# Performance work log

Measured on AMD Instinct MI355X. Metric: run time of the kernel, lower is better.

The kernel has to match this reference:

```python
import jax, jax.numpy as jnp
import numpy as np

B, T, C = 2, 2048, 2048
N_HEAD, N_KV_HEAD = 16, 4
HEAD_DIM = C // N_HEAD  # 128
HALF = HEAD_DIM // 2    # 64


def _rms_norm(x):
    # F.rms_norm with no weight: x / sqrt(mean(x^2) + eps), eps = dtype eps
    eps = jnp.finfo(x.dtype).eps
    return x * jax.lax.rsqrt(jnp.mean(x * x, axis=-1, keepdims=True) + eps)


def _rope_apply(x, cos, sin):
    # x: [B, H, T, Hs]; cos/sin: [1, 1, T, Hs/2]
    x1, x2 = x[..., :HALF], x[..., HALF:]
    return jnp.concatenate([x1 * cos - x2 * sin, x1 * sin + x2 * cos], axis=-1)


def setup_inputs() -> dict:
    key = jax.random.key(0)
    ks = jax.random.split(key, 8)
    x = jax.random.normal(ks[0], (B, T, C), dtype=jnp.float32)
    # real RoPE tables (base 10000), shape [1,1,T,HALF]
    inv_freq = 1.0 / (10000.0 ** (np.arange(0, HALF, dtype=np.float32) / HALF))
    t = np.arange(T, dtype=np.float32)
    ang = np.einsum('t,f->tf', t, inv_freq)
    cos = jnp.asarray(np.cos(ang))[None, None]
    sin = jnp.asarray(np.sin(ang))[None, None]
    s = 0.02
    Wq = jax.random.normal(ks[1], (C, N_HEAD * HEAD_DIM), dtype=jnp.float32) * s
    Wk = jax.random.normal(ks[2], (C, N_KV_HEAD * HEAD_DIM), dtype=jnp.float32) * s
    Wv = jax.random.normal(ks[3], (C, N_KV_HEAD * HEAD_DIM), dtype=jnp.float32) * s
    Wo = jax.random.normal(ks[4], (C, C), dtype=jnp.float32) * s
    bo = jnp.zeros((C,), dtype=jnp.float32)
    return {"x": x, "cos": cos, "sin": sin, "Wq": Wq, "Wk": Wk, "Wv": Wv, "Wo": Wo, "bo": bo}


def reference(x, cos, sin, Wq, Wk, Wv, Wo, bo):
    Bq, Tq, Cq = x.shape
    G = N_HEAD // N_KV_HEAD
    # QKV projections (GQA, no bias)
    q = (x @ Wq).reshape(Bq, Tq, N_HEAD, HEAD_DIM)
    k = (x @ Wk).reshape(Bq, Tq, N_KV_HEAD, HEAD_DIM)
    v = (x @ Wv).reshape(Bq, Tq, N_KV_HEAD, HEAD_DIM)
    # QK RMSNorm (over head_dim), then to [B, H, T, Hs]
    q = jnp.transpose(_rms_norm(q), (0, 2, 1, 3))
    k = jnp.transpose(_rms_norm(k), (0, 2, 1, 3))
    v = jnp.transpose(v, (0, 2, 1, 3))
    # RoPE
    q = _rope_apply(q, cos[:, :, :Tq, :], sin[:, :, :Tq, :])
    k = _rope_apply(k, cos[:, :, :Tq, :], sin[:, :, :Tq, :])
    # GQA: repeat kv heads across groups
    k = jnp.repeat(k, G, axis=1)  # [B, H, T, Hs]
    v = jnp.repeat(v, G, axis=1)
    # Causal SDPA
    scale = 1.0 / jnp.sqrt(jnp.asarray(HEAD_DIM, dtype=x.dtype))
    scores = jnp.einsum('bhqd,bhkd->bhqk', q, k) * scale
    causal = jnp.tril(jnp.ones((Tq, Tq), dtype=bool))
    scores = jnp.where(causal, scores, jnp.asarray(-jnp.inf, dtype=scores.dtype))
    attn = jax.nn.softmax(scores, axis=-1)
    y = jnp.einsum('bhqk,bhkd->bhqd', attn, v)
    y = jnp.transpose(y, (0, 2, 1, 3)).reshape(Bq, Tq, Cq)
    return y @ Wo + bo
```

## Files before the change

kernel.cpp:

```cpp
#include <hip/hip_runtime.h>
#include <hip/hip_bf16.h>
#include <math.h>

#define BB 2
#define TT 2048
#define CC 2048
#define NH 16
#define NKV 4
#define HD 128
#define HALF 64
#define MTOT (BB*TT)
#define NQKV (CC + 2*NKV*HD)

typedef unsigned short u16;
typedef __attribute__((ext_vector_type(8))) short bf16x8;
typedef __attribute__((ext_vector_type(4))) float f32x4;

__device__ __forceinline__ u16 f2bf(float f) {
  unsigned u = __float_as_uint(f);
  unsigned r = (u + 0x7FFFu + ((u >> 16) & 1u)) >> 16;
  return (u16)r;
}
__device__ __forceinline__ float bf2f(u16 v) {
  return __uint_as_float(((unsigned)v) << 16);
}

__device__ __forceinline__ void gl_lds16(const void* g, void* l) {
  __builtin_amdgcn_global_load_lds(
      (const __attribute__((address_space(1))) unsigned int*)g,
      (__attribute__((address_space(3))) unsigned int*)l, 16, 0, 0);
}

__global__ __launch_bounds__(256) void prep(
    const float* __restrict__ x, const float* __restrict__ Wq,
    const float* __restrict__ Wk, const float* __restrict__ Wv,
    const float* __restrict__ Wo, u16* __restrict__ xb,
    u16* __restrict__ Wt, u16* __restrict__ Wot) {
  const int z = blockIdx.z;
  const int tx = threadIdx.x, ty = threadIdx.y;
  if (z == 4) {
    const int tid = ty * 32 + tx;
    const int i = (blockIdx.y * 64 + blockIdx.x) * 256 + tid;
    const float4* s4 = (const float4*)x;
    float4 a = s4[(size_t)i * 2], b = s4[(size_t)i * 2 + 1];
    bf16x8 o;
    o[0] = (short)f2bf(a.x); o[1] = (short)f2bf(a.y);
    o[2] = (short)f2bf(a.z); o[3] = (short)f2bf(a.w);
    o[4] = (short)f2bf(b.x); o[5] = (short)f2bf(b.y);
    o[6] = (short)f2bf(b.z); o[7] = (short)f2bf(b.w);
    ((bf16x8*)xb)[i] = o;
    return;
  }
  const float* W; u16* dst; int N; int row_off;
  if (z == 0)      { W = Wq; dst = Wt;  N = 2048; row_off = 0; }
  else if (z == 1) { W = Wk; dst = Wt;  N = 512;  row_off = 2048; }
  else if (z == 2) { W = Wv; dst = Wt;  N = 512;  row_off = 2560; }
  else             { W = Wo; dst = Wot; N = 2048; row_off = 0; }
  const int n0 = blockIdx.x * 32, k0 = blockIdx.y * 32;
  if (n0 >= N) return;
  __shared__ float tile[32][33];
#pragma unroll
  for (int i = 0; i < 4; ++i)
    tile[ty + 8 * i][tx] = W[(size_t)(k0 + ty + 8 * i) * N + n0 + tx];
  __syncthreads();
#pragma unroll
  for (int i = 0; i < 4; ++i)
    dst[(size_t)(row_off + n0 + ty + 8 * i) * CC + k0 + tx] =
        f2bf(tile[tx][ty + 8 * i]);
}

__global__ __launch_bounds__(256) void gemm_bt_bf16(
    const u16* __restrict__ A, const u16* __restrict__ Bt,
    const float* __restrict__ bias, float* __restrict__ C,
    int M, int N, int K, int out_bf16) {
  __shared__ u16 As[128 * 32];
  __shared__ u16 Bs[128 * 32];
  const int tid = threadIdx.x;
  const int wave = tid >> 6, lane = tid & 63;
  const int quad = lane >> 4, lo = lane & 15;
  const int bm = blockIdx.y * 128, bn = blockIdx.x * 128;
  const int wm = (wave & 1) * 64, wn = (wave >> 1) * 64;

  f32x4 acc[4][4];
#pragma unroll
  for (int i = 0; i < 4; ++i)
#pragma unroll
    for (int j = 0; j < 4; ++j)
#pragma unroll
      for (int r = 0; r < 4; ++r) acc[i][j][r] = 0.f;

  const int iss0 = wave * 2, iss1 = wave * 2 + 1;
  const int e0 = iss0 * 512 + lane * 8, e1 = iss1 * 512 + lane * 8;
  const int r0 = e0 >> 5, c0 = e0 & 31;
  const int r1 = e1 >> 5, c1 = e1 & 31;

  for (int k0 = 0; k0 < K; k0 += 32) {
    gl_lds16(A + (size_t)(bm + r0) * K + k0 + c0, (char*)As + iss0 * 1024);
    gl_lds16(A + (size_t)(bm + r1) * K + k0 + c1, (char*)As + iss1 * 1024);
    gl_lds16(Bt + (size_t)(bn + r0) * K + k0 + c0, (char*)Bs + iss0 * 1024);
    gl_lds16(Bt + (size_t)(bn + r1) * K + k0 + c1, (char*)Bs + iss1 * 1024);
    __syncthreads();

    bf16x8 af[4], bg[4];
#pragma unroll
    for (int i = 0; i < 4; ++i)
      af[i] = *(const bf16x8*)&As[(wm + i * 16 + lo) * 32 + quad * 8];
#pragma unroll
    for (int j = 0; j < 4; ++j)
      bg[j] = *(const bf16x8*)&Bs[(wn + j * 16 + lo) * 32 + quad * 8];
#pragma unroll
    for (int i = 0; i < 4; ++i)
#pragma unroll
      for (int j = 0; j < 4; ++j)
        acc[i][j] = __builtin_amdgcn_mfma_f32_16x16x32_bf16(af[i], bg[j], acc[i][j], 0, 0, 0);
    __syncthreads();
  }

#pragma unroll
  for (int i = 0; i < 4; ++i)
#pragma unroll
    for (int j = 0; j < 4; ++j)
#pragma unroll
      for (int r = 0; r < 4; ++r) {
        int row = bm + wm + i * 16 + quad * 4 + r;
        int col = bn + wn + j * 16 + lo;
        float v = acc[i][j][r];
        if (bias) v += bias[col];
        if (out_bf16) ((u16*)C)[(size_t)row * N + col] = f2bf(v);
        else          C[(size_t)row * N + col] = v;
      }
}

__global__ __launch_bounds__(256) void qkv_post(
    const u16* __restrict__ qkv_lin, const float* __restrict__ cosp,
    const float* __restrict__ sinp, u16* __restrict__ q, u16* __restrict__ k) {
  const int bt = blockIdx.x;
  const int hh = blockIdx.y * 4 + (threadIdx.x >> 6);
  const int lane = threadIdx.x & 63;
  const int t = bt & (TT - 1), b = bt >> 11;
  const int col = (hh < NH) ? hh * HD : CC + (hh - NH) * HD;
  const u16* src = qkv_lin + (size_t)bt * NQKV + col;
  float v1 = bf2f(src[lane]), v2 = bf2f(src[lane + 64]);
  float ss = v1 * v1 + v2 * v2;
#pragma unroll
  for (int mm = 1; mm < 64; mm <<= 1) ss += __shfl_xor(ss, mm, 64);
  float rms = rsqrtf(ss * (1.f / 128.f) + 1.1920929e-7f);
  float c = cosp[t * HALF + lane], s = sinp[t * HALF + lane];
  float o1 = v1 * rms * c - v2 * rms * s;
  float o2 = v1 * rms * s + v2 * rms * c;
  if (hh < NH) {
    u16* dst = q + (((size_t)(b * NH + hh)) * TT + t) * HD;
    dst[lane] = f2bf(o1); dst[lane + 64] = f2bf(o2);
  } else {
    u16* dst = k + (((size_t)(b * NKV + (hh - NH))) * TT + t) * HD;
    dst[lane] = f2bf(o1); dst[lane + 64] = f2bf(o2);
  }
}

__global__ __launch_bounds__(256) void v_transpose(
    const u16* __restrict__ qkv_lin, u16* __restrict__ vt) {
  __shared__ u16 tile[32][33];
  const int t0 = blockIdx.x * 32, d0 = blockIdx.y * 32;
  const int p = blockIdx.z;
  const int b = p >> 2, kv = p & 3;
  const int tx = threadIdx.x, ty = threadIdx.y;
#pragma unroll
  for (int i = 0; i < 4; ++i)
    tile[ty + 8 * i][tx] =
        qkv_lin[(size_t)(b * TT + t0 + ty + 8 * i) * NQKV + CC + NKV * HD + kv * HD + d0 + tx];
  __syncthreads();
  const int tperm = ((tx >> 2) & 3) * 8 + (tx & 3) + 4 * ((tx >> 4) & 1);
#pragma unroll
  for (int i = 0; i < 4; ++i)
    vt[((size_t)p * HD + d0 + ty + 8 * i) * TT + t0 + tperm] = tile[tx][ty + 8 * i];
}

__device__ __forceinline__ void softmax_pack(
    const f32x4* sacc, float& l_lane, bf16x8* ap, int rowq, int t0,
    bool diag, int quad) {
  const float cc = 0.12751744050808612f;
  float e[4][4];
  if (diag) {
#pragma unroll
    for (int ct = 0; ct < 4; ++ct)
#pragma unroll
      for (int r = 0; r < 4; ++r) {
        float v = __builtin_amdgcn_exp2f(sacc[ct][r] * cc);
        if (t0 + ct * 16 + quad * 4 + r > rowq) v = 0.f;
        l_lane += v; e[ct][r] = v;
      }
  } else {
#pragma unroll
    for (int ct = 0; ct < 4; ++ct)
#pragma unroll
      for (int r = 0; r < 4; ++r) {
        float v = __builtin_amdgcn_exp2f(sacc[ct][r] * cc);
        l_lane += v; e[ct][r] = v;
      }
  }
#pragma unroll
  for (int k2 = 0; k2 < 2; ++k2) {
    bf16x8 ch;
#pragma unroll
    for (int j = 0; j < 8; ++j)
      ch[j] = (short)f2bf(e[k2 * 2 + (j >> 2)][j & 3]);
    ap[k2] = ch;
  }
}

__global__ __launch_bounds__(256, 2) void attn_mfma(
    const u16* __restrict__ Qb, const u16* __restrict__ Kb,
    const u16* __restrict__ Vt, u16* __restrict__ Y) {
  __shared__ u16 Ks[2][8192];
  __shared__ u16 Vs[2][8192];

  const int qt = blockIdx.x;
  const int bh = blockIdx.y;
  const int b = bh >> 4, h = bh & 15, kvh = h >> 2;
  const int tid = threadIdx.x;
  const int wave = tid >> 6, lane = tid & 63;
  const int quad = lane >> 4, lo = lane & 15;

  const int rowsA = qt * 64, rowsB = (31 - qt) * 64;
  const u16* Qg = Qb + (size_t)(b * NH + h) * TT * HD;
  const u16* Kg = Kb + (size_t)(b * NKV + kvh) * TT * HD;
  const u16* Vg = Vt + (size_t)(b * NKV + kvh) * HD * TT;

  bf16x8 aq[2][4];
#pragma unroll
  for (int kc = 0; kc < 4; ++kc) {
    aq[0][kc] = *(const bf16x8*)(Qg + (size_t)(rowsA + wave * 16 + lo) * HD + kc * 32 + quad * 8);
    aq[1][kc] = *(const bf16x8*)(Qg + (size_t)(rowsB + wave * 16 + lo) * HD + kc * 32 + quad * 8);
  }

  const u16* kgp[4]; const u16* vgp[4];
  u16* klp[2][4]; u16* vlp[2][4];
#pragma unroll
  for (int c = 0; c < 4; ++c) {
    const int s = wave * 4 + c;
    const int ct = s >> 2, kq = s & 3;
    kgp[c] = Kg + (size_t)(ct * 16 + lo) * HD + kq * 32 + quad * 8;
    const int dt = s >> 1, k2 = s & 1;
    vgp[c] = Vg + (size_t)(dt * 16 + lo) * TT + k2 * 32 + quad * 8;
    klp[0][c] = &Ks[0][s * 512]; klp[1][c] = &Ks[1][s * 512];
    vlp[0][c] = &Vs[0][s * 512]; vlp[1][c] = &Vs[1][s * 512];
  }

  f32x4 oacc[2][8];
#pragma unroll
  for (int rb = 0; rb < 2; ++rb)
#pragma unroll
    for (int dt = 0; dt < 8; ++dt)
#pragma unroll
      for (int r = 0; r < 4; ++r) oacc[rb][dt][r] = 0.f;
  float l_lane[2] = {0.f, 0.f};

  const int ntiles = 32 - qt;
  const int rowqA = rowsA + wave * 16 + lo;
  const int rowqB = rowsB + wave * 16 + lo;

#pragma unroll
  for (int c = 0; c < 4; ++c) {
    gl_lds16(kgp[c], klp[0][c]); kgp[c] += 64 * HD;
    gl_lds16(vgp[c], vlp[0][c]); vgp[c] += 64;
  }

  for (int nt = 0; nt < ntiles; ++nt) {
    const int par = nt & 1;
    __syncthreads();
    if (nt + 1 < ntiles) {
#pragma unroll
      for (int c = 0; c < 4; ++c) {
        gl_lds16(kgp[c], klp[par ^ 1][c]); kgp[c] += 64 * HD;
        gl_lds16(vgp[c], vlp[par ^ 1][c]); vgp[c] += 64;
      }
    }
    const u16* ksb = Ks[par];
    const u16* vsb = Vs[par];
    const int t0 = nt * 64;
    const bool act0 = (nt <= qt);

    f32x4 sacc[2][4];
#pragma unroll
    for (int rb = 0; rb < 2; ++rb)
#pragma unroll
      for (int ct = 0; ct < 4; ++ct)
#pragma unroll
        for (int r = 0; r < 4; ++r) sacc[rb][ct][r] = 0.f;
#pragma unroll
    for (int ct = 0; ct < 4; ++ct)
#pragma unroll
      for (int kc = 0; kc < 4; ++kc) {
        bf16x8 bk = *(const bf16x8*)&ksb[(ct * 4 + kc) * 512 + lane * 8];
        sacc[1][ct] = __builtin_amdgcn_mfma_f32_16x16x32_bf16(bk, aq[1][kc], sacc[1][ct], 0, 0, 0);
        if (act0)
          sacc[0][ct] = __builtin_amdgcn_mfma_f32_16x16x32_bf16(bk, aq[0][kc], sacc[0][ct], 0, 0, 0);
      }

    bf16x8 ap[2][2];
    softmax_pack(sacc[1], l_lane[1], ap[1], rowqB, t0,
                 t0 + 63 > rowsB + wave * 16, quad);
    if (act0)
      softmax_pack(sacc[0], l_lane[0], ap[0], rowqA, t0,
                   t0 + 63 > rowsA + wave * 16, quad);

#pragma unroll
    for (int dt = 0; dt < 8; ++dt)
#pragma unroll
      for (int k2 = 0; k2 < 2; ++k2) {
        bf16x8 bv = *(const bf16x8*)&vsb[(dt * 2 + k2) * 512 + lane * 8];
        oacc[1][dt] = __builtin_amdgcn_mfma_f32_16x16x32_bf16(ap[1][k2], bv, oacc[1][dt], 0, 0, 0);
        if (act0)
          oacc[0][dt] = __builtin_amdgcn_mfma_f32_16x16x32_bf16(ap[0][k2], bv, oacc[0][dt], 0, 0, 0);
      }
  }

  float linv[2][4];
#pragma unroll
  for (int rb = 0; rb < 2; ++rb) {
    float l = l_lane[rb];
    l += __shfl_xor(l, 16, 64);
    l += __shfl_xor(l, 32, 64);
    l = 1.f / l;
#pragma unroll
    for (int r = 0; r < 4; ++r)
      linv[rb][r] = __shfl(l, quad * 4 + r, 64);
  }
#pragma unroll
  for (int rb = 0; rb < 2; ++rb) {
    const int rows = (rb == 0) ? rowsA : rowsB;
    const size_t row0 = (size_t)b * TT + rows + wave * 16 + quad * 4;
#pragma unroll
    for (int dt = 0; dt < 8; ++dt)
#pragma unroll
      for (int r = 0; r < 4; ++r)
        Y[(row0 + r) * CC + h * HD + dt * 16 + lo] = f2bf(oacc[rb][dt][r] * linv[rb][r]);
  }
}

extern "C" void kernel_launch(void* const* d_in, const int* in_sizes, int n_in,
                              void* d_out, int out_size, void* d_ws, size_t ws_size,
                              hipStream_t stream) {
  (void)in_sizes; (void)n_in; (void)out_size; (void)ws_size;
  const float* x    = (const float*)d_in[0];
  const float* cosp = (const float*)d_in[1];
  const float* sinp = (const float*)d_in[2];
  const float* Wq   = (const float*)d_in[3];
  const float* Wk   = (const float*)d_in[4];
  const float* Wv   = (const float*)d_in[5];
  const float* Wo   = (const float*)d_in[6];
  const float* bo   = (const float*)d_in[7];
  float* out = (float*)d_out;
  char* ws = (char*)d_ws;

  const size_t MB = 1024 * 1024;
  u16* xb      = (u16*)(ws);
  u16* Wt      = (u16*)(ws + 16 * MB);
  u16* qkv_lin = (u16*)(ws + 28 * MB);
  u16* Wot     = (u16*)(ws + 52 * MB);
  u16* qb_buf  = (u16*)(ws);
  u16* kb      = (u16*)(ws + 16 * MB);
  u16* vt      = (u16*)(ws + 20 * MB);
  u16* y       = (u16*)(ws + 28 * MB);

  prep<<<dim3(64, 64, 5), dim3(32, 8), 0, stream>>>(x, Wq, Wk, Wv, Wo, xb, Wt, Wot);

  gemm_bt_bf16<<<dim3(NQKV / 128, MTOT / 128), 256, 0, stream>>>(
      xb, Wt, nullptr, (float*)qkv_lin, MTOT, NQKV, CC, 1);

  qkv_post<<<dim3(MTOT, 5), 256, 0, stream>>>(qkv_lin, cosp, sinp, qb_buf, kb);

  v_transpose<<<dim3(TT / 32, HD / 32, BB * NKV), dim3(32, 8), 0, stream>>>(qkv_lin, vt);

  attn_mfma<<<dim3(16, BB * NH), 256, 0, stream>>>(qb_buf, kb, vt, y);

  gemm_bt_bf16<<<dim3(CC / 128, MTOT / 128), 256, 0, stream>>>(
      y, Wot, bo, out, MTOT, CC, CC, 0);
}
```

Measured before the change: 341.7 us.

## Replace GEMM with 256x256 double-buffered 8-wave pipelined MFMA kernel

Replaces the 128x128 single-buffered GEMM with a 256x256 tile, 512-thread kernel. It uses K=64 steps, double-buffered LDS with an XOR swizzle, and direct global-to-LDS loads interleaved across four MFMA phases with barriers and s_setprio. The goal is to hide global load latency behind MFMA work, raise data reuse per tile, and avoid LDS bank conflicts. In exchange, the grid shrinks to far fewer blocks (e.g. 12x16 for QKV, 8x16 for the output projection), which may underfill the CUs, and register and LDS pressure goes up.

```diff
diff --git a/kernel.cpp b/kernel.cpp
--- a/kernel.cpp
+++ b/kernel.cpp
@@ -69,66 +69,165 @@
         f2bf(tile[tx][ty + 8 * i]);
 }
 
-__global__ __launch_bounds__(256) void gemm_bt_bf16(
+__global__ __launch_bounds__(512, 2) void gemm_8ph(
     const u16* __restrict__ A, const u16* __restrict__ Bt,
     const float* __restrict__ bias, float* __restrict__ C,
     int M, int N, int K, int out_bf16) {
-  __shared__ u16 As[128 * 32];
-  __shared__ u16 Bs[128 * 32];
+  __shared__ u16 As[32768];
+  __shared__ u16 Bs[32768];
   const int tid = threadIdx.x;
-  const int wave = tid >> 6, lane = tid & 63;
+  const int w = tid >> 6, lane = tid & 63;
   const int quad = lane >> 4, lo = lane & 15;
-  const int bm = blockIdx.y * 128, bn = blockIdx.x * 128;
-  const int wm = (wave & 1) * 64, wn = (wave >> 1) * 64;
-
-  f32x4 acc[4][4];
-#pragma unroll
-  for (int i = 0; i < 4; ++i)
-#pragma unroll
-    for (int j = 0; j < 4; ++j)
-#pragma unroll
-      for (int r = 0; r < 4; ++r) acc[i][j][r] = 0.f;
-
-  const int iss0 = wave * 2, iss1 = wave * 2 + 1;
-  const int e0 = iss0 * 512 + lane * 8, e1 = iss1 * 512 + lane * 8;
-  const int r0 = e0 >> 5, c0 = e0 & 31;
-  const int r1 = e1 >> 5, c1 = e1 & 31;
-
-  for (int k0 = 0; k0 < K; k0 += 32) {
-    gl_lds16(A + (size_t)(bm + r0) * K + k0 + c0, (char*)As + iss0 * 1024);
-    gl_lds16(A + (size_t)(bm + r1) * K + k0 + c1, (char*)As + iss1 * 1024);
-    gl_lds16(Bt + (size_t)(bn + r0) * K + k0 + c0, (char*)Bs + iss0 * 1024);
-    gl_lds16(Bt + (size_t)(bn + r1) * K + k0 + c1, (char*)Bs + iss1 * 1024);
-    __syncthreads();
-
-    bf16x8 af[4], bg[4];
+  const int wm = w >> 2, wn = w & 3;
+  const int bm = blockIdx.y * 256, bn = blockIdx.x * 256;
+  const int NT = K >> 6;
+
+  const u16* agp[2][2]; const u16* bgp[2][2];
+#pragma unroll
+  for (int h = 0; h < 2; ++h)
+#pragma unroll
+    for (int j = 0; j < 2; ++j) {
+      const unsigned X = (unsigned)h * 16384u +
+                         (unsigned)((w * 2 + j) * 64 + lane) * 16u;
+      const int row = (int)(X >> 7);
+      const int ce = (int)(((X & 127u) ^ (((X >> 9) & 3u) << 5)) >> 1);
+      agp[h][j] = A  + (size_t)(bm + row) * K + ce;
+      bgp[h][j] = Bt + (size_t)(bn + row) * K + ce;
+    }
+  char* const lAs = (char*)As;
+  char* const lBs = (char*)Bs;
+  const int woff = w * 2048;
+
+#define STGA(hh, bufp, kt) do { \
+    gl_lds16(agp[hh][0] + (size_t)(kt) * 64, lAs + (bufp) * 32768 + (hh) * 16384 + woff); \
+    gl_lds16(agp[hh][1] + (size_t)(kt) * 64, lAs + (bufp) * 32768 + (hh) * 16384 + woff + 1024); \
+  } while (0)
+#define STGB(hh, bufp, kt) do { \
+    gl_lds16(bgp[hh][0] + (size_t)(kt) * 64, lBs + (bufp) * 32768 + (hh) * 16384 + woff); \
+    gl_lds16(bgp[hh][1] + (size_t)(kt) * 64, lBs + (bufp) * 32768 + (hh) * 16384 + woff + 1024); \
+  } while (0)
+
+  const int sw  = ((lo >> 2) & 3) << 5;
+  const int co0 = (quad * 16) ^ sw;
+  const int co1 = (64 + quad * 16) ^ sw;
+  const int aRB = (wm * 128 + lo) * 128;
+  const int bRB = (wn * 64 + lo) * 128;
+
+  f32x4 acc[8][4];
+#pragma unroll
+  for (int ri = 0; ri < 8; ++ri)
+#pragma unroll
+    for (int ci = 0; ci < 4; ++ci)
+#pragma unroll
+      for (int r = 0; r < 4; ++r) acc[ri][ci][r] = 0.f;
+
+  STGA(0, 0, 0); STGA(1, 0, 0); STGB(0, 0, 0); STGB(1, 0, 0);
+  STGB(0, 1, 1); STGB(1, 1, 1); STGA(0, 1, 1);
+  asm volatile("s_waitcnt vmcnt(6)" ::: "memory");
+  __builtin_amdgcn_s_barrier();
+
+  for (int t = 0; t < NT; ++t) {
+    const int pa = t & 1;
+    const char* Ab = lAs + pa * 32768 + aRB;
+    const char* Bb = lBs + pa * 32768 + bRB;
+    bf16x8 a[4][2], b0[2][2], b1[2][2];
+
+#pragma unroll
+    for (int i = 0; i < 4; ++i) {
+      a[i][0] = *(const bf16x8*)(Ab + i * 2048 + co0);
+      a[i][1] = *(const bf16x8*)(Ab + i * 2048 + co1);
+    }
+#pragma unroll
+    for (int j = 0; j < 2; ++j) {
+      b0[j][0] = *(const bf16x8*)(Bb + j * 2048 + co0);
+      b0[j][1] = *(const bf16x8*)(Bb + j * 2048 + co1);
+    }
+    if (t + 1 < NT) STGA(1, (t + 1) & 1, t + 1);
+    __builtin_amdgcn_s_barrier();
+    asm volatile("s_waitcnt lgkmcnt(0)");
+    __builtin_amdgcn_s_setprio(1);
 #pragma unroll
     for (int i = 0; i < 4; ++i)
-      af[i] = *(const bf16x8*)&As[(wm + i * 16 + lo) * 32 + quad * 8];
-#pragma unroll
-    for (int j = 0; j < 4; ++j)
-      bg[j] = *(const bf16x8*)&Bs[(wn + j * 16 + lo) * 32 + quad * 8];
+#pragma unroll
+      for (int j = 0; j < 2; ++j) {
+        acc[i][j] = __builtin_amdgcn_mfma_f32_16x16x32_bf16(a[i][0], b0[j][0], acc[i][j], 0, 0, 0);
+        acc[i][j] = __builtin_amdgcn_mfma_f32_16x16x32_bf16(a[i][1], b0[j][1], acc[i][j], 0, 0, 0);
+      }
+    __builtin_amdgcn_s_setprio(0);
+    __builtin_amdgcn_s_barrier();
+
+#pragma unroll
+    for (int j = 0; j < 2; ++j) {
+      b1[j][0] = *(const bf16x8*)(Bb + 4096 + j * 2048 + co0);
+      b1[j][1] = *(const bf16x8*)(Bb + 4096 + j * 2048 + co1);
+    }
+    __builtin_amdgcn_s_barrier();
+    asm volatile("s_waitcnt lgkmcnt(0)");
+    __builtin_amdgcn_s_setprio(1);
 #pragma unroll
     for (int i = 0; i < 4; ++i)
 #pragma unroll
-      for (int j = 0; j < 4; ++j)
-        acc[i][j] = __builtin_amdgcn_mfma_f32_16x16x32_bf16(af[i], bg[j], acc[i][j], 0, 0, 0);
-    __syncthreads();
-  }
-
-#pragma unroll
-  for (int i = 0; i < 4; ++i)
-#pragma unroll
-    for (int j = 0; j < 4; ++j)
+      for (int j = 0; j < 2; ++j) {
+        acc[i][2 + j] = __builtin_amdgcn_mfma_f32_16x16x32_bf16(a[i][0], b1[j][0], acc[i][2 + j], 0, 0, 0);
+        acc[i][2 + j] = __builtin_amdgcn_mfma_f32_16x16x32_bf16(a[i][1], b1[j][1], acc[i][2 + j], 0, 0, 0);
+      }
+    __builtin_amdgcn_s_setprio(0);
+    __builtin_amdgcn_s_barrier();
+
+#pragma unroll
+    for (int i = 0; i < 4; ++i) {
+      a[i][0] = *(const bf16x8*)(Ab + 8192 + i * 2048 + co0);
+      a[i][1] = *(const bf16x8*)(Ab + 8192 + i * 2048 + co1);
+    }
+    if (t + 2 < NT) STGB(0, pa, t + 2);
+    __builtin_amdgcn_s_barrier();
+    asm volatile("s_waitcnt lgkmcnt(0)");
+    __builtin_amdgcn_s_setprio(1);
+#pragma unroll
+    for (int i = 0; i < 4; ++i)
+#pragma unroll
+      for (int j = 0; j < 2; ++j) {
+        acc[4 + i][2 + j] = __builtin_amdgcn_mfma_f32_16x16x32_bf16(a[i][0], b1[j][0], acc[4 + i][2 + j], 0, 0, 0);
+        acc[4 + i][2 + j] = __builtin_amdgcn_mfma_f32_16x16x32_bf16(a[i][1], b1[j][1], acc[4 + i][2 + j], 0, 0, 0);
+      }
+    __builtin_amdgcn_s_setprio(0);
+    __builtin_amdgcn_s_barrier();
+
+    if (t + 2 < NT) { STGB(1, pa, t + 2); STGA(0, pa, t + 2); }
+    if (t + 2 < NT)      asm volatile("s_waitcnt vmcnt(6)" ::: "memory");
+    else if (t + 1 < NT) asm volatile("s_waitcnt vmcnt(0)" ::: "memory");
+    __builtin_amdgcn_s_barrier();
+    asm volatile("s_waitcnt lgkmcnt(0)");
+    __builtin_amdgcn_s_setprio(1);
+#pragma unroll
+    for (int i = 0; i < 4; ++i)
+#pragma unroll
+      for (int j = 0; j < 2; ++j) {
+        acc[4 + i][j] = __builtin_amdgcn_mfma_f32_16x16x32_bf16(a[i][0], b0[j][0], acc[4 + i][j], 0, 0, 0);
+        acc[4 + i][j] = __builtin_amdgcn_mfma_f32_16x16x32_bf16(a[i][1], b0[j][1], acc[4 + i][j], 0, 0, 0);
+      }
+    __builtin_amdgcn_s_setprio(0);
+    __builtin_amdgcn_s_barrier();
+  }
+#undef STGA
+#undef STGB
+
+  const int rbase = bm + wm * 128;
+  const int cbase = bn + wn * 64;
+#pragma unroll
+  for (int ri = 0; ri < 8; ++ri)
+#pragma unroll
+    for (int ci = 0; ci < 4; ++ci) {
+      const int col = cbase + ci * 16 + lo;
+      const float bv = bias ? bias[col] : 0.f;
 #pragma unroll
       for (int r = 0; r < 4; ++r) {
-        int row = bm + wm + i * 16 + quad * 4 + r;
-        int col = bn + wn + j * 16 + lo;
-        float v = acc[i][j][r];
-        if (bias) v += bias[col];
+        const int row = rbase + ri * 16 + quad * 4 + r;
+        const float v = acc[ri][ci][r] + bv;
         if (out_bf16) ((u16*)C)[(size_t)row * N + col] = f2bf(v);
         else          C[(size_t)row * N + col] = v;
       }
+    }
 }
 
 __global__ __launch_bounds__(256) void qkv_post(
@@ -365,7 +464,7 @@
 
   prep<<<dim3(64, 64, 5), dim3(32, 8), 0, stream>>>(x, Wq, Wk, Wv, Wo, xb, Wt, Wot);
 
-  gemm_bt_bf16<<<dim3(NQKV / 128, MTOT / 128), 256, 0, stream>>>(
+  gemm_8ph<<<dim3(NQKV / 256, MTOT / 256), 512, 0, stream>>>(
       xb, Wt, nullptr, (float*)qkv_lin, MTOT, NQKV, CC, 1);
 
   qkv_post<<<dim3(MTOT, 5), 256, 0, stream>>>(qkv_lin, cosp, sinp, qb_buf, kb);
@@ -374,6 +473,6 @@
 
   attn_mfma<<<dim3(16, BB * NH), 256, 0, stream>>>(qb_buf, kb, vt, y);
 
-  gemm_bt_bf16<<<dim3(CC / 128, MTOT / 128), 256, 0, stream>>>(
+  gemm_8ph<<<dim3(CC / 256, MTOT / 256), 512, 0, stream>>>(
       y, Wot, bo, out, MTOT, CC, CC, 0);
 }
```

New measurement: 344.7 us. About the same (+0.9%).
